# Kernel optimization log

Hardware: AMD Instinct MI355X
Metric: run time of the kernel (lower is better)

## Reference

```python
import jax, jax.numpy as jnp
import numpy as np

D = 1024   # embedding_dim
H = 16     # head_num
DH = D // H
STD = 0.02


def setup_inputs() -> dict:
    key = jax.random.key(0)
    ks = jax.random.split(key, 8)
    B, S = 16, 2048
    inp = {
        "hidden_states": jax.random.normal(ks[0], (B, S, D), dtype=jnp.float32),
        "attention_mask": jnp.zeros((B, 1, S), dtype=jnp.float32),
        # nn.Linear params, stored as [in, out] for direct matmul
        "Wq": jax.random.normal(ks[1], (D, D), dtype=jnp.float32) * STD,
        "bq": jnp.zeros((D,), dtype=jnp.float32),
        "Wqa": jax.random.normal(ks[2], (D, H), dtype=jnp.float32) * STD,
        "bqa": jnp.zeros((H,), dtype=jnp.float32),
        "Wk": jax.random.normal(ks[3], (D, D), dtype=jnp.float32) * STD,
        "bk": jnp.zeros((D,), dtype=jnp.float32),
        "Wka": jax.random.normal(ks[4], (D, H), dtype=jnp.float32) * STD,
        "bka": jnp.zeros((H,), dtype=jnp.float32),
        "Wt": jax.random.normal(ks[5], (D, D), dtype=jnp.float32) * STD,
        "bt": jnp.zeros((D,), dtype=jnp.float32),
    }
    return inp


def reference(hidden_states, attention_mask, Wq, bq, Wqa, bqa, Wk, bk, Wka, bka, Wt, bt):
    B, S, _ = hidden_states.shape
    scale = 1.0 / np.sqrt(DH).astype(np.float32)

    mixed_q = hidden_states @ Wq + bq          # [B,S,D]
    mixed_k = hidden_states @ Wk + bk          # [B,S,D]

    # per-head query pooling scores: [B,S,H] -> [B,H,S]
    q_score = jnp.transpose(mixed_q @ Wqa + bqa, (0, 2, 1)) * scale + attention_mask
    q_weight = jax.nn.softmax(q_score, axis=-1)                 # [B,H,S]

    q_layer = mixed_q.reshape(B, S, H, DH).transpose(0, 2, 1, 3)  # [B,H,S,dh]
    pooled_q = jnp.einsum('bhs,bhsd->bhd', q_weight, q_layer)     # [B,H,dh]
    pooled_q_flat = pooled_q.reshape(B, 1, D)                     # [B,1,D] (head-major)

    # elementwise modulate keys with pooled query (broadcast, no repeat)
    mixed_qk = mixed_k * pooled_q_flat                            # [B,S,D]

    qk_score = jnp.transpose(mixed_qk @ Wka + bka, (0, 2, 1)) * scale + attention_mask
    qk_weight = jax.nn.softmax(qk_score, axis=-1)                 # [B,H,S]

    k_layer = mixed_qk.reshape(B, S, H, DH).transpose(0, 2, 1, 3)  # [B,H,S,dh]
    pooled_k = jnp.einsum('bhs,bhsd->bhd', qk_weight, k_layer)     # [B,H,dh]

    weighted = pooled_k[:, :, None, :] * q_layer                   # [B,H,S,dh]
    weighted = weighted.transpose(0, 2, 1, 3).reshape(B, S, D)     # [B,S,D]

    return weighted @ Wt + bt + mixed_q
```

## Files before the change

kernel.cpp:

```cpp
#include <hip/hip_runtime.h>
#include <hip/hip_bf16.h>
#include <stdint.h>

#define D_ 1024
#define H_ 16
#define DH_ 64
#define S_ 2048
#define B_ 16
static constexpr float SCALE = 0.125f;

typedef __bf16 bf16_t;
typedef __bf16 bf16x8 __attribute__((ext_vector_type(8)));
typedef __bf16 bf16x4 __attribute__((ext_vector_type(4)));
typedef float  f32x4  __attribute__((ext_vector_type(4)));

__device__ __forceinline__ void llds16(const void* g, void* l) {
  __builtin_amdgcn_global_load_lds(
      (const __attribute__((address_space(1))) void*)g,
      (__attribute__((address_space(3))) void*)l, 16, 0, 0);
}

__global__ __launch_bounds__(256)
void f32_to_bf16(const float* __restrict__ src, bf16_t* __restrict__ dst) {
  size_t base = ((size_t)blockIdx.x * 256 + threadIdx.x) * 8;
  f32x4 a = *(const f32x4*)&src[base];
  f32x4 b = *(const f32x4*)&src[base + 4];
  bf16x8 o;
#pragma unroll
  for (int i = 0; i < 4; ++i) { o[i] = (bf16_t)a[i]; o[4 + i] = (bf16_t)b[i]; }
  *(bf16x8*)&dst[base] = o;
}

__global__ __launch_bounds__(256)
void transpose1024_all(const float* __restrict__ s0, const float* __restrict__ s1,
                       const float* __restrict__ s2, bf16_t* __restrict__ d0,
                       bf16_t* __restrict__ d1, bf16_t* __restrict__ d2) {
  __shared__ bf16_t t[64][65];
  const float* src = (blockIdx.z == 0) ? s0 : (blockIdx.z == 1) ? s1 : s2;
  bf16_t* dst      = (blockIdx.z == 0) ? d0 : (blockIdx.z == 1) ? d1 : d2;
  const int n0 = blockIdx.x * 64, k0 = blockIdx.y * 64;
  const int r = threadIdx.x >> 4, c4 = (threadIdx.x & 15) * 4;
#pragma unroll
  for (int p = 0; p < 4; ++p) {
    int row = p * 16 + r;
    f32x4 f = *(const f32x4*)&src[(size_t)(k0 + row) * 1024 + n0 + c4];
#pragma unroll
    for (int i = 0; i < 4; ++i) t[row][c4 + i] = (bf16_t)f[i];
  }
  __syncthreads();
#pragma unroll
  for (int p = 0; p < 4; ++p) {
    int row = p * 16 + r;
    bf16x4 v;
#pragma unroll
    for (int i = 0; i < 4; ++i) v[i] = t[c4 + i][row];
    *(bf16x4*)&dst[(size_t)(n0 + row) * 1024 + k0 + c4] = v;
  }
}

__global__ __launch_bounds__(256)
void transpose_small_all(const float* __restrict__ sa, const float* __restrict__ sb,
                         bf16_t* __restrict__ da, bf16_t* __restrict__ db) {
  int g = blockIdx.x * 256 + threadIdx.x;
  const float* src = (g < 1024) ? sa : sb;
  bf16_t* dst      = (g < 1024) ? da : db;
  int k = g & 1023;
#pragma unroll
  for (int h = 0; h < H_; ++h) dst[h * 1024 + k] = (bf16_t)src[k * H_ + h];
}

template <int MODE>
__global__ __launch_bounds__(256, 2)
void gemm_bt(const bf16_t* __restrict__ A, const bf16_t* __restrict__ BT,
             const float* __restrict__ bias, void* __restrict__ Cout,
             const float* __restrict__ pscale, const bf16_t* __restrict__ resid,
             const float* __restrict__ pkA) {
  constexpr int K = 1024, N = 1024;
  __shared__ __align__(16) bf16_t lA[128 * 32];
  __shared__ __align__(16) bf16_t lB[128 * 32];
  __shared__ __align__(16) float est[4][16 * 68];
  const int tid = threadIdx.x;
  const int lane = tid & 63, wid = tid >> 6;
  const int wr = wid >> 1, wc = wid & 1;

  const int wgid = (blockIdx.x & 7) * 256 + (blockIdx.x >> 3);
  const int m0 = (wgid >> 3) * 128;
  const int n0 = (wgid & 7) * 128;
  const int b = m0 / S_;

  const int ar = lane & 15;
  const int kq = lane >> 4;

  int rowc[2], colc[2], dstoff[2];
#pragma unroll
  for (int j = 0; j < 2; ++j) {
    int c = j * 256 + tid;
    int row = c >> 2, s = c & 3;
    rowc[j] = row;
    colc[j] = (((s - (row >> 1)) & 3) << 3);
    dstoff[j] = c * 8;
  }

  f32x4 acc[4][4] = {};

  for (int k0 = 0; k0 < K; k0 += 32) {
#pragma unroll
    for (int j = 0; j < 2; ++j) {
      const bf16_t* gb = BT + (size_t)(n0 + rowc[j]) * K + k0 + colc[j];
      llds16(gb, lB + dstoff[j]);
      if (MODE == 2) {
        bf16x8 v = *(const bf16x8*)(A + (size_t)(m0 + rowc[j]) * K + k0 + colc[j]);
        const float* pkp = pkA + b * D_ + k0 + colc[j];
        f32x4 p0 = *(const f32x4*)pkp;
        f32x4 p1 = *(const f32x4*)(pkp + 4);
        bf16x8 o;
#pragma unroll
        for (int i = 0; i < 4; ++i) {
          o[i]     = (bf16_t)((float)v[i] * p0[i]);
          o[4 + i] = (bf16_t)((float)v[4 + i] * p1[i]);
        }
        *(bf16x8*)&lA[dstoff[j]] = o;
      } else {
        const bf16_t* ga = A + (size_t)(m0 + rowc[j]) * K + k0 + colc[j];
        llds16(ga, lA + dstoff[j]);
      }
    }
    __syncthreads();
    bf16x8 af[4], bg[4];
#pragma unroll
    for (int m = 0; m < 4; ++m) {
      int r = wr * 64 + m * 16 + ar;
      af[m] = *(const bf16x8*)&lA[r * 32 + (((kq + (r >> 1)) & 3) << 3)];
    }
#pragma unroll
    for (int n = 0; n < 4; ++n) {
      int r = wc * 64 + n * 16 + ar;
      bg[n] = *(const bf16x8*)&lB[r * 32 + (((kq + (r >> 1)) & 3) << 3)];
    }
#pragma unroll
    for (int m = 0; m < 4; ++m)
#pragma unroll
      for (int n = 0; n < 4; ++n)
        acc[m][n] = __builtin_amdgcn_mfma_f32_16x16x32_bf16(af[m], bg[n], acc[m][n], 0, 0, 0);
    __syncthreads();
  }

  float* st = est[wid];
  const int erow = lane >> 2;
  const int ecol = (lane & 3) * 16;
  const int gcb = n0 + wc * 64;
  const int qrow = (lane >> 4) * 4;
  const int qcol = lane & 15;
  f32x4 bb[4], ps[4];
#pragma unroll
  for (int q = 0; q < 4; ++q) bb[q] = *(const f32x4*)&bias[gcb + ecol + q * 4];
  if (MODE == 1) {
#pragma unroll
    for (int q = 0; q < 4; ++q) ps[q] = *(const f32x4*)&pscale[b * D_ + gcb + ecol + q * 4];
  }
#pragma unroll
  for (int m = 0; m < 4; ++m) {
#pragma unroll
    for (int n = 0; n < 4; ++n)
#pragma unroll
      for (int j = 0; j < 4; ++j)
        st[(qrow + j) * 68 + n * 16 + qcol] = acc[m][n][j];
    asm volatile("s_waitcnt lgkmcnt(0)" ::: "memory");
    __builtin_amdgcn_sched_barrier(0);
    const int grow = m0 + wr * 64 + m * 16 + erow;
    f32x4 v[4];
#pragma unroll
    for (int q = 0; q < 4; ++q) v[q] = *(f32x4*)&st[erow * 68 + ecol + q * 4];
#pragma unroll
    for (int q = 0; q < 4; ++q)
#pragma unroll
      for (int i = 0; i < 4; ++i) v[q][i] += bb[q][i];
    if (MODE == 1) {
#pragma unroll
      for (int q = 0; q < 4; ++q)
#pragma unroll
        for (int i = 0; i < 4; ++i) v[q][i] *= ps[q][i];
    }
    if (MODE == 2) {
      bf16x8 r0 = *(const bf16x8*)&resid[(size_t)grow * N + gcb + ecol];
      bf16x8 r1 = *(const bf16x8*)&resid[(size_t)grow * N + gcb + ecol + 8];
#pragma unroll
      for (int i = 0; i < 4; ++i) { v[0][i] += (float)r0[i]; v[1][i] += (float)r0[4 + i]; }
#pragma unroll
      for (int i = 0; i < 4; ++i) { v[2][i] += (float)r1[i]; v[3][i] += (float)r1[4 + i]; }
      float* op = (float*)Cout + (size_t)grow * N + gcb + ecol;
#pragma unroll
      for (int q = 0; q < 4; ++q) *(f32x4*)&op[q * 4] = v[q];
    } else {
      bf16x8 o0, o1;
#pragma unroll
      for (int i = 0; i < 4; ++i) { o0[i] = (bf16_t)v[0][i]; o0[4 + i] = (bf16_t)v[1][i]; }
#pragma unroll
      for (int i = 0; i < 4; ++i) { o1[i] = (bf16_t)v[2][i]; o1[4 + i] = (bf16_t)v[3][i]; }
      bf16_t* op = (bf16_t*)Cout + (size_t)grow * N + gcb + ecol;
      *(bf16x8*)&op[0] = o0;
      *(bf16x8*)&op[8] = o1;
    }
  }
}

__global__ __launch_bounds__(256)
void score_kernel(const bf16_t* __restrict__ X, const bf16_t* __restrict__ WaT,
                  const float* __restrict__ ba, const float* __restrict__ mask,
                  float* __restrict__ scores) {
  const int lane = threadIdx.x & 63, wid = threadIdx.x >> 6;
  const int m0 = blockIdx.x * 64 + wid * 16;
  const int ar = lane & 15, ak = (lane >> 4) * 8;
  f32x4 acc = {};
  for (int k0 = 0; k0 < D_; k0 += 32) {
    bf16x8 a = *(const bf16x8*)&X[(size_t)(m0 + ar) * D_ + k0 + ak];
    bf16x8 b = *(const bf16x8*)&WaT[(size_t)ar * D_ + k0 + ak];
    acc = __builtin_amdgcn_mfma_f32_16x16x32_bf16(a, b, acc, 0, 0, 0);
  }
  const int h = lane & 15;
  const int srow = m0 + (lane >> 4) * 4;
  const int bb = srow / S_;
  const int s0 = srow - bb * S_;
  const float bah = ba[h];
  f32x4 mv = *(const f32x4*)&mask[(size_t)bb * S_ + s0];
  f32x4 outv;
#pragma unroll
  for (int j = 0; j < 4; ++j)
    outv[j] = (acc[j] + bah) * SCALE + mv[j];
  *(f32x4*)&scores[((size_t)(bb * H_ + h)) * S_ + s0] = outv;
}

__global__ __launch_bounds__(256)
void softmax_rows(const float* __restrict__ scores, float* __restrict__ wout) {
  __shared__ float rA[4], rB[4];
  const int tid = threadIdx.x, lane = tid & 63, wid = tid >> 6;
  const float* srow = scores + (size_t)blockIdx.x * S_;
  float* wrow = wout + (size_t)blockIdx.x * S_;
  f32x4 v0 = *(const f32x4*)&srow[tid * 4];
  f32x4 v1 = *(const f32x4*)&srow[1024 + tid * 4];
  float mx = fmaxf(fmaxf(fmaxf(v0[0], v0[1]), fmaxf(v0[2], v0[3])),
                   fmaxf(fmaxf(v1[0], v1[1]), fmaxf(v1[2], v1[3])));
#pragma unroll
  for (int o = 32; o; o >>= 1) mx = fmaxf(mx, __shfl_xor(mx, o));
  if (lane == 0) rA[wid] = mx;
  __syncthreads();
  mx = fmaxf(fmaxf(rA[0], rA[1]), fmaxf(rA[2], rA[3]));
  float sum = 0.f;
#pragma unroll
  for (int i = 0; i < 4; ++i) { v0[i] = __expf(v0[i] - mx); sum += v0[i]; }
#pragma unroll
  for (int i = 0; i < 4; ++i) { v1[i] = __expf(v1[i] - mx); sum += v1[i]; }
#pragma unroll
  for (int o = 32; o; o >>= 1) sum += __shfl_xor(sum, o);
  if (lane == 0) rB[wid] = sum;
  __syncthreads();
  sum = rB[0] + rB[1] + rB[2] + rB[3];
  const float inv = 1.0f / sum;
#pragma unroll
  for (int i = 0; i < 4; ++i) { v0[i] *= inv; v1[i] *= inv; }
  *(f32x4*)&wrow[tid * 4] = v0;
  *(f32x4*)&wrow[1024 + tid * 4] = v1;
}

__global__ __launch_bounds__(256)
void pool_partial(const bf16_t* __restrict__ X, const float* __restrict__ w,
                  float* __restrict__ partials) {
  __shared__ float sm[2][1024];
  const int tid = threadIdx.x;
  const int chunk = blockIdx.x, b = blockIdx.y;
  const int s0 = chunk * 32;
  const int dc = (tid & 127) * 8;
  const int sp = tid >> 7;
  const int h = dc >> 6;
  const float* wrow = w + ((size_t)b * H_ + h) * S_ + s0;
  const bf16_t* Xb = X + ((size_t)b * S_ + s0) * D_ + dc;
  float acc[8] = {};
  for (int s = sp; s < 32; s += 2) {
    bf16x8 xv = *(const bf16x8*)&Xb[(size_t)s * D_];
    float wt = wrow[s];
#pragma unroll
    for (int j = 0; j < 8; ++j) acc[j] += wt * (float)xv[j];
  }
#pragma unroll
  for (int j = 0; j < 8; ++j) sm[sp][dc + j] = acc[j];
  __syncthreads();
  const int d0 = tid * 4;
  f32x4 r;
#pragma unroll
  for (int j = 0; j < 4; ++j) r[j] = sm[0][d0 + j] + sm[1][d0 + j];
  *(f32x4*)&partials[((size_t)chunk * B_ + b) * D_ + d0] = r;
}

__global__ __launch_bounds__(256)
void pool_reduce(const float* __restrict__ partials, float* __restrict__ pooled) {
  const int idx = blockIdx.x * 256 + threadIdx.x;
  float s = 0.f;
#pragma unroll 8
  for (int c = 0; c < 64; ++c) s += partials[(size_t)c * (B_ * D_) + idx];
  pooled[idx] = s;
}

extern "C" void kernel_launch(void* const* d_in, const int* in_sizes, int n_in,
                              void* d_out, int out_size, void* d_ws, size_t ws_size,
                              hipStream_t stream) {
  const float* hs   = (const float*)d_in[0];
  const float* mask = (const float*)d_in[1];
  const float* Wq   = (const float*)d_in[2];
  const float* bq   = (const float*)d_in[3];
  const float* Wqa  = (const float*)d_in[4];
  const float* bqa  = (const float*)d_in[5];
  const float* Wk   = (const float*)d_in[6];
  const float* bk   = (const float*)d_in[7];
  const float* Wka  = (const float*)d_in[8];
  const float* bka  = (const float*)d_in[9];
  const float* Wt   = (const float*)d_in[10];
  const float* bt   = (const float*)d_in[11];

  char* ws = (char*)d_ws;
  float*  pq    = (float*)(ws + (64u << 10));
  float*  pk    = (float*)(ws + (128u << 10));
  bf16_t* WqaT  = (bf16_t*)(ws + (1u << 20));
  bf16_t* WkaT  = (bf16_t*)(ws + (1u << 20) + 32768);
  bf16_t* WqT   = (bf16_t*)(ws + (2u << 20));
  bf16_t* WkT   = (bf16_t*)(ws + (4u << 20));
  bf16_t* WtT   = (bf16_t*)(ws + (6u << 20));
  bf16_t* hsb   = (bf16_t*)(ws + (8u << 20));
  bf16_t* mq    = (bf16_t*)(ws + (8u << 20) + ((size_t)64 << 20));
  bf16_t* mqk   = (bf16_t*)(ws + (8u << 20) + ((size_t)128 << 20));
  float* scores = (float*)(ws + (8u << 20) + ((size_t)192 << 20));
  float* wsm    = (float*)(ws + (8u << 20) + ((size_t)194 << 20));
  float* parts  = (float*)(ws + (8u << 20) + ((size_t)196 << 20));

  f32_to_bf16<<<16384, 256, 0, stream>>>(hs, hsb);
  transpose1024_all<<<dim3(16, 16, 3), 256, 0, stream>>>(Wq, Wk, Wt, WqT, WkT, WtT);
  transpose_small_all<<<8, 256, 0, stream>>>(Wqa, Wka, WqaT, WkaT);

  gemm_bt<0><<<2048, 256, 0, stream>>>(hsb, WqT, bq, mq, nullptr, nullptr, nullptr);

  score_kernel<<<512, 256, 0, stream>>>(mq, WqaT, bqa, mask, scores);
  softmax_rows<<<256, 256, 0, stream>>>(scores, wsm);
  pool_partial<<<dim3(64, 16), 256, 0, stream>>>(mq, wsm, parts);
  pool_reduce<<<64, 256, 0, stream>>>(parts, pq);

  gemm_bt<1><<<2048, 256, 0, stream>>>(hsb, WkT, bk, mqk, pq, nullptr, nullptr);

  score_kernel<<<512, 256, 0, stream>>>(mqk, WkaT, bka, mask, scores);
  softmax_rows<<<256, 256, 0, stream>>>(scores, wsm);
  pool_partial<<<dim3(64, 16), 256, 0, stream>>>(mqk, wsm, parts);
  pool_reduce<<<64, 256, 0, stream>>>(parts, pk);

  gemm_bt<2><<<2048, 256, 0, stream>>>(mq, WtT, bt, d_out, nullptr, mq, pk);
}
```

Baseline: 398.6 us.

## Fuse Q and K projections into one GEMM, defer pooled-query scaling

The Q and K projection GEMMs are merged into one 4096-block launch that computes unscaled mixed_k alongside mixed_q. The multiplication by pooled_q moves into the key score kernel, which scales its A operand on the fly, and into pool_reduce, which scales the pooled sum by pq. Because pooling is linear, the weighted sum of mk times pq equals the weighted sum of mqk. This removes the serial dependency of the K GEMM on the query pooling chain and lets both large GEMMs run as one bigger launch. The score kernel gains per-element scaling loads, and rounding changes slightly because mk is stored in bf16 before the scale is applied.

```diff
diff --git a/kernel.cpp b/kernel.cpp
--- a/kernel.cpp
+++ b/kernel.cpp
@@ -69,12 +69,11 @@
   for (int h = 0; h < H_; ++h) dst[h * 1024 + k] = (bf16_t)src[k * H_ + h];
 }
 
-template <int MODE>
 __global__ __launch_bounds__(256, 2)
-void gemm_bt(const bf16_t* __restrict__ A, const bf16_t* __restrict__ BT,
-             const float* __restrict__ bias, void* __restrict__ Cout,
-             const float* __restrict__ pscale, const bf16_t* __restrict__ resid,
-             const float* __restrict__ pkA) {
+void gemm_qk(const bf16_t* __restrict__ A, const bf16_t* __restrict__ WqT,
+             const bf16_t* __restrict__ WkT, const float* __restrict__ bq,
+             const float* __restrict__ bk, bf16_t* __restrict__ mq,
+             bf16_t* __restrict__ mk) {
   constexpr int K = 1024, N = 1024;
   __shared__ __align__(16) bf16_t lA[128 * 32];
   __shared__ __align__(16) bf16_t lB[128 * 32];
@@ -83,10 +82,13 @@
   const int lane = tid & 63, wid = tid >> 6;
   const int wr = wid >> 1, wc = wid & 1;
 
-  const int wgid = (blockIdx.x & 7) * 256 + (blockIdx.x >> 3);
-  const int m0 = (wgid >> 3) * 128;
-  const int n0 = (wgid & 7) * 128;
-  const int b = m0 / S_;
+  const int wgid = (blockIdx.x & 7) * 512 + (blockIdx.x >> 3);
+  const int m0 = (wgid >> 4) * 128;
+  const int nsel = wgid & 15;
+  const int n0 = (nsel & 7) * 128;
+  const bf16_t* BT = (nsel < 8) ? WqT : WkT;
+  const float* bias = (nsel < 8) ? bq : bk;
+  bf16_t* Cout = (nsel < 8) ? mq : mk;
 
   const int ar = lane & 15;
   const int kq = lane >> 4;
@@ -106,24 +108,8 @@
   for (int k0 = 0; k0 < K; k0 += 32) {
 #pragma unroll
     for (int j = 0; j < 2; ++j) {
-      const bf16_t* gb = BT + (size_t)(n0 + rowc[j]) * K + k0 + colc[j];
-      llds16(gb, lB + dstoff[j]);
-      if (MODE == 2) {
-        bf16x8 v = *(const bf16x8*)(A + (size_t)(m0 + rowc[j]) * K + k0 + colc[j]);
-        const float* pkp = pkA + b * D_ + k0 + colc[j];
-        f32x4 p0 = *(const f32x4*)pkp;
-        f32x4 p1 = *(const f32x4*)(pkp + 4);
-        bf16x8 o;
-#pragma unroll
-        for (int i = 0; i < 4; ++i) {
-          o[i]     = (bf16_t)((float)v[i] * p0[i]);
-          o[4 + i] = (bf16_t)((float)v[4 + i] * p1[i]);
-        }
-        *(bf16x8*)&lA[dstoff[j]] = o;
-      } else {
-        const bf16_t* ga = A + (size_t)(m0 + rowc[j]) * K + k0 + colc[j];
-        llds16(ga, lA + dstoff[j]);
-      }
+      llds16(BT + (size_t)(n0 + rowc[j]) * K + k0 + colc[j], lB + dstoff[j]);
+      llds16(A + (size_t)(m0 + rowc[j]) * K + k0 + colc[j], lA + dstoff[j]);
     }
     __syncthreads();
     bf16x8 af[4], bg[4];
@@ -151,13 +137,9 @@
   const int gcb = n0 + wc * 64;
   const int qrow = (lane >> 4) * 4;
   const int qcol = lane & 15;
-  f32x4 bb[4], ps[4];
+  f32x4 bb[4];
 #pragma unroll
   for (int q = 0; q < 4; ++q) bb[q] = *(const f32x4*)&bias[gcb + ecol + q * 4];
-  if (MODE == 1) {
-#pragma unroll
-    for (int q = 0; q < 4; ++q) ps[q] = *(const f32x4*)&pscale[b * D_ + gcb + ecol + q * 4];
-  }
 #pragma unroll
   for (int m = 0; m < 4; ++m) {
 #pragma unroll
@@ -175,51 +157,152 @@
     for (int q = 0; q < 4; ++q)
 #pragma unroll
       for (int i = 0; i < 4; ++i) v[q][i] += bb[q][i];
-    if (MODE == 1) {
-#pragma unroll
-      for (int q = 0; q < 4; ++q)
-#pragma unroll
-        for (int i = 0; i < 4; ++i) v[q][i] *= ps[q][i];
-    }
-    if (MODE == 2) {
-      bf16x8 r0 = *(const bf16x8*)&resid[(size_t)grow * N + gcb + ecol];
-      bf16x8 r1 = *(const bf16x8*)&resid[(size_t)grow * N + gcb + ecol + 8];
-#pragma unroll
-      for (int i = 0; i < 4; ++i) { v[0][i] += (float)r0[i]; v[1][i] += (float)r0[4 + i]; }
-#pragma unroll
-      for (int i = 0; i < 4; ++i) { v[2][i] += (float)r1[i]; v[3][i] += (float)r1[4 + i]; }
-      float* op = (float*)Cout + (size_t)grow * N + gcb + ecol;
-#pragma unroll
-      for (int q = 0; q < 4; ++q) *(f32x4*)&op[q * 4] = v[q];
-    } else {
-      bf16x8 o0, o1;
-#pragma unroll
-      for (int i = 0; i < 4; ++i) { o0[i] = (bf16_t)v[0][i]; o0[4 + i] = (bf16_t)v[1][i]; }
-#pragma unroll
-      for (int i = 0; i < 4; ++i) { o1[i] = (bf16_t)v[2][i]; o1[4 + i] = (bf16_t)v[3][i]; }
-      bf16_t* op = (bf16_t*)Cout + (size_t)grow * N + gcb + ecol;
-      *(bf16x8*)&op[0] = o0;
-      *(bf16x8*)&op[8] = o1;
-    }
-  }
-}
-
+    bf16x8 o0, o1;
+#pragma unroll
+    for (int i = 0; i < 4; ++i) { o0[i] = (bf16_t)v[0][i]; o0[4 + i] = (bf16_t)v[1][i]; }
+#pragma unroll
+    for (int i = 0; i < 4; ++i) { o1[i] = (bf16_t)v[2][i]; o1[4 + i] = (bf16_t)v[3][i]; }
+    bf16_t* op = Cout + (size_t)grow * N + gcb + ecol;
+    *(bf16x8*)&op[0] = o0;
+    *(bf16x8*)&op[8] = o1;
+  }
+}
+
+__global__ __launch_bounds__(256, 2)
+void gemm_out(const bf16_t* __restrict__ A, const bf16_t* __restrict__ BT,
+              const float* __restrict__ bias, float* __restrict__ Cout,
+              const bf16_t* __restrict__ resid, const float* __restrict__ pkA) {
+  constexpr int K = 1024, N = 1024;
+  __shared__ __align__(16) bf16_t lA[128 * 32];
+  __shared__ __align__(16) bf16_t lB[128 * 32];
+  __shared__ __align__(16) float est[4][16 * 68];
+  const int tid = threadIdx.x;
+  const int lane = tid & 63, wid = tid >> 6;
+  const int wr = wid >> 1, wc = wid & 1;
+
+  const int wgid = (blockIdx.x & 7) * 256 + (blockIdx.x >> 3);
+  const int m0 = (wgid >> 3) * 128;
+  const int n0 = (wgid & 7) * 128;
+  const int b = m0 / S_;
+
+  const int ar = lane & 15;
+  const int kq = lane >> 4;
+
+  int rowc[2], colc[2], dstoff[2];
+#pragma unroll
+  for (int j = 0; j < 2; ++j) {
+    int c = j * 256 + tid;
+    int row = c >> 2, s = c & 3;
+    rowc[j] = row;
+    colc[j] = (((s - (row >> 1)) & 3) << 3);
+    dstoff[j] = c * 8;
+  }
+
+  f32x4 acc[4][4] = {};
+
+  for (int k0 = 0; k0 < K; k0 += 32) {
+#pragma unroll
+    for (int j = 0; j < 2; ++j) {
+      llds16(BT + (size_t)(n0 + rowc[j]) * K + k0 + colc[j], lB + dstoff[j]);
+      bf16x8 v = *(const bf16x8*)(A + (size_t)(m0 + rowc[j]) * K + k0 + colc[j]);
+      const float* pkp = pkA + b * D_ + k0 + colc[j];
+      f32x4 p0 = *(const f32x4*)pkp;
+      f32x4 p1 = *(const f32x4*)(pkp + 4);
+      bf16x8 o;
+#pragma unroll
+      for (int i = 0; i < 4; ++i) {
+        o[i]     = (bf16_t)((float)v[i] * p0[i]);
+        o[4 + i] = (bf16_t)((float)v[4 + i] * p1[i]);
+      }
+      *(bf16x8*)&lA[dstoff[j]] = o;
+    }
+    __syncthreads();
+    bf16x8 af[4], bg[4];
+#pragma unroll
+    for (int m = 0; m < 4; ++m) {
+      int r = wr * 64 + m * 16 + ar;
+      af[m] = *(const bf16x8*)&lA[r * 32 + (((kq + (r >> 1)) & 3) << 3)];
+    }
+#pragma unroll
+    for (int n = 0; n < 4; ++n) {
+      int r = wc * 64 + n * 16 + ar;
+      bg[n] = *(const bf16x8*)&lB[r * 32 + (((kq + (r >> 1)) & 3) << 3)];
+    }
+#pragma unroll
+    for (int m = 0; m < 4; ++m)
+#pragma unroll
+      for (int n = 0; n < 4; ++n)
+        acc[m][n] = __builtin_amdgcn_mfma_f32_16x16x32_bf16(af[m], bg[n], acc[m][n], 0, 0, 0);
+    __syncthreads();
+  }
+
+  float* st = est[wid];
+  const int erow = lane >> 2;
+  const int ecol = (lane & 3) * 16;
+  const int gcb = n0 + wc * 64;
+  const int qrow = (lane >> 4) * 4;
+  const int qcol = lane & 15;
+  f32x4 bb[4];
+#pragma unroll
+  for (int q = 0; q < 4; ++q) bb[q] = *(const f32x4*)&bias[gcb + ecol + q * 4];
+#pragma unroll
+  for (int m = 0; m < 4; ++m) {
+#pragma unroll
+    for (int n = 0; n < 4; ++n)
+#pragma unroll
+      for (int j = 0; j < 4; ++j)
+        st[(qrow + j) * 68 + n * 16 + qcol] = acc[m][n][j];
+    asm volatile("s_waitcnt lgkmcnt(0)" ::: "memory");
+    __builtin_amdgcn_sched_barrier(0);
+    const int grow = m0 + wr * 64 + m * 16 + erow;
+    f32x4 v[4];
+#pragma unroll
+    for (int q = 0; q < 4; ++q) v[q] = *(f32x4*)&st[erow * 68 + ecol + q * 4];
+#pragma unroll
+    for (int q = 0; q < 4; ++q)
+#pragma unroll
+      for (int i = 0; i < 4; ++i) v[q][i] += bb[q][i];
+    bf16x8 r0 = *(const bf16x8*)&resid[(size_t)grow * N + gcb + ecol];
+    bf16x8 r1 = *(const bf16x8*)&resid[(size_t)grow * N + gcb + ecol + 8];
+#pragma unroll
+    for (int i = 0; i < 4; ++i) { v[0][i] += (float)r0[i]; v[1][i] += (float)r0[4 + i]; }
+#pragma unroll
+    for (int i = 0; i < 4; ++i) { v[2][i] += (float)r1[i]; v[3][i] += (float)r1[4 + i]; }
+    float* op = Cout + (size_t)grow * N + gcb + ecol;
+#pragma unroll
+    for (int q = 0; q < 4; ++q) *(f32x4*)&op[q * 4] = v[q];
+  }
+}
+
+template <int SCALED>
 __global__ __launch_bounds__(256)
 void score_kernel(const bf16_t* __restrict__ X, const bf16_t* __restrict__ WaT,
                   const float* __restrict__ ba, const float* __restrict__ mask,
-                  float* __restrict__ scores) {
+                  const float* __restrict__ pq, float* __restrict__ scores) {
   const int lane = threadIdx.x & 63, wid = threadIdx.x >> 6;
   const int m0 = blockIdx.x * 64 + wid * 16;
   const int ar = lane & 15, ak = (lane >> 4) * 8;
+  const int bb = m0 >> 11;
   f32x4 acc = {};
   for (int k0 = 0; k0 < D_; k0 += 32) {
     bf16x8 a = *(const bf16x8*)&X[(size_t)(m0 + ar) * D_ + k0 + ak];
+    if (SCALED) {
+      const float* pp = pq + bb * D_ + k0 + ak;
+      f32x4 p0 = *(const f32x4*)pp;
+      f32x4 p1 = *(const f32x4*)(pp + 4);
+      bf16x8 a2;
+#pragma unroll
+      for (int i = 0; i < 4; ++i) {
+        a2[i]     = (bf16_t)((float)a[i] * p0[i]);
+        a2[4 + i] = (bf16_t)((float)a[4 + i] * p1[i]);
+      }
+      a = a2;
+    }
     bf16x8 b = *(const bf16x8*)&WaT[(size_t)ar * D_ + k0 + ak];
     acc = __builtin_amdgcn_mfma_f32_16x16x32_bf16(a, b, acc, 0, 0, 0);
   }
   const int h = lane & 15;
   const int srow = m0 + (lane >> 4) * 4;
-  const int bb = srow / S_;
   const int s0 = srow - bb * S_;
   const float bah = ba[h];
   f32x4 mv = *(const f32x4*)&mask[(size_t)bb * S_ + s0];
@@ -291,12 +374,15 @@
   *(f32x4*)&partials[((size_t)chunk * B_ + b) * D_ + d0] = r;
 }
 
-__global__ __launch_bounds__(256)
-void pool_reduce(const float* __restrict__ partials, float* __restrict__ pooled) {
+template <int SCALED>
+__global__ __launch_bounds__(256)
+void pool_reduce(const float* __restrict__ partials, const float* __restrict__ pq,
+                 float* __restrict__ pooled) {
   const int idx = blockIdx.x * 256 + threadIdx.x;
   float s = 0.f;
 #pragma unroll 8
   for (int c = 0; c < 64; ++c) s += partials[(size_t)c * (B_ * D_) + idx];
+  if (SCALED) s *= pq[idx];
   pooled[idx] = s;
 }
 
@@ -326,7 +412,7 @@
   bf16_t* WtT   = (bf16_t*)(ws + (6u << 20));
   bf16_t* hsb   = (bf16_t*)(ws + (8u << 20));
   bf16_t* mq    = (bf16_t*)(ws + (8u << 20) + ((size_t)64 << 20));
-  bf16_t* mqk   = (bf16_t*)(ws + (8u << 20) + ((size_t)128 << 20));
+  bf16_t* mk    = (bf16_t*)(ws + (8u << 20) + ((size_t)128 << 20));
   float* scores = (float*)(ws + (8u << 20) + ((size_t)192 << 20));
   float* wsm    = (float*)(ws + (8u << 20) + ((size_t)194 << 20));
   float* parts  = (float*)(ws + (8u << 20) + ((size_t)196 << 20));
@@ -335,19 +421,17 @@
   transpose1024_all<<<dim3(16, 16, 3), 256, 0, stream>>>(Wq, Wk, Wt, WqT, WkT, WtT);
   transpose_small_all<<<8, 256, 0, stream>>>(Wqa, Wka, WqaT, WkaT);
 
-  gemm_bt<0><<<2048, 256, 0, stream>>>(hsb, WqT, bq, mq, nullptr, nullptr, nullptr);
-
-  score_kernel<<<512, 256, 0, stream>>>(mq, WqaT, bqa, mask, scores);
+  gemm_qk<<<4096, 256, 0, stream>>>(hsb, WqT, WkT, bq, bk, mq, mk);
+
+  score_kernel<0><<<512, 256, 0, stream>>>(mq, WqaT, bqa, mask, nullptr, scores);
   softmax_rows<<<256, 256, 0, stream>>>(scores, wsm);
   pool_partial<<<dim3(64, 16), 256, 0, stream>>>(mq, wsm, parts);
-  pool_reduce<<<64, 256, 0, stream>>>(parts, pq);
-
-  gemm_bt<1><<<2048, 256, 0, stream>>>(hsb, WkT, bk, mqk, pq, nullptr, nullptr);
-
-  score_kernel<<<512, 256, 0, stream>>>(mqk, WkaT, bka, mask, scores);
+  pool_reduce<0><<<64, 256, 0, stream>>>(parts, nullptr, pq);
+
+  score_kernel<1><<<512, 256, 0, stream>>>(mk, WkaT, bka, mask, pq, scores);
   softmax_rows<<<256, 256, 0, stream>>>(scores, wsm);
-  pool_partial<<<dim3(64, 16), 256, 0, stream>>>(mqk, wsm, parts);
-  pool_reduce<<<64, 256, 0, stream>>>(parts, pk);
-
-  gemm_bt<2><<<2048, 256, 0, stream>>>(mq, WtT, bt, d_out, nullptr, mq, pk);
-}
+  pool_partial<<<dim3(64, 16), 256, 0, stream>>>(mk, wsm, parts);
+  pool_reduce<1><<<64, 256, 0, stream>>>(parts, pq, pk);
+
+  gemm_out<<<2048, 256, 0, stream>>>(mq, WtT, bt, (float*)d_out, mq, pk);
+}
```

Result: no change. 400.2 us (+0.4%).
